# Kernel tuning notes

Measured on AMD Instinct MI355X. Metric: run time of the kernel, lower is better.

The kernel has to match this reference:

```python
import jax, jax.numpy as jnp
import numpy as np

N = 50000
E = 600000
D = 128
BN_EPS = 1e-5


def _gcn_layer(x, src, dst, ew, W, b, n):
    # x: [N, Din] -> [N, Dout]; PyG GCNConv: linear, symmetric norm (self-loops
    # already appended to src/dst/ew by caller), gather, scatter-add, bias.
    h = x @ W  # [N, Dout]
    deg = jax.ops.segment_sum(ew, dst, num_segments=n)  # [N]
    dinv = jnp.where(deg > 0, jax.lax.rsqrt(jnp.maximum(deg, 1e-30)), 0.0)
    norm = dinv[src] * ew * dinv[dst]  # [E+N]
    msg = h[src] * norm[:, None]  # [E+N, Dout] -- dominant memory traffic
    out = jax.ops.segment_sum(msg, dst, num_segments=n)
    return out + b


def _bn_eval(x, gamma, beta, mean, var):
    return (x - mean) * jax.lax.rsqrt(var + BN_EPS) * gamma + beta


def setup_inputs() -> dict:
    key = jax.random.key(0)
    ks = jax.random.split(key, 16)
    s = 1.0 / np.sqrt(D)
    inp = {
        "x": jax.random.normal(ks[0], (N, D), dtype=jnp.float32),
        "edge_index": jax.random.randint(ks[1], (2, E), 0, N, dtype=jnp.int32),
        "edge_weight": jax.random.uniform(ks[2], (E,), dtype=jnp.float32),
        "W0": jax.random.uniform(ks[3], (D, D), jnp.float32, -s, s),
        "b0": jnp.zeros((D,), jnp.float32),
        "W1": jax.random.uniform(ks[4], (D, D), jnp.float32, -s, s),
        "b1": jnp.zeros((D,), jnp.float32),
        "gamma0": jnp.ones((D,), jnp.float32),
        "beta0": jnp.zeros((D,), jnp.float32),
        "mean0": 0.1 * jax.random.normal(ks[5], (D,), jnp.float32),
        "var0": jax.random.uniform(ks[6], (D,), jnp.float32, 0.5, 1.5),
        "gamma1": jnp.ones((D,), jnp.float32),
        "beta1": jnp.zeros((D,), jnp.float32),
        "mean1": 0.1 * jax.random.normal(ks[7], (D,), jnp.float32),
        "var1": jax.random.uniform(ks[8], (D,), jnp.float32, 0.5, 1.5),
        "act_params": jnp.ones((2,), jnp.float32),  # activation_params init = ones(num_layers)
    }
    return inp


def reference(x, edge_index, edge_weight, W0, b0, W1, b1, gamma0, beta0, mean0, var0, gamma1, beta1, mean1, var1, act_params):
    # Add self-loops with weight 1 (PyG gcn_norm fill_value=1), shared by both layers.
    loop = jnp.arange(N, dtype=edge_index.dtype)
    src = jnp.concatenate([edge_index[0], loop])
    dst = jnp.concatenate([edge_index[1], loop])
    ew = jnp.concatenate([edge_weight, jnp.ones((N,), edge_weight.dtype)])

    # layer 0: conv -> BN (eval: running stats) -> adaptive ReLU/GELU blend
    h = _gcn_layer(x, src, dst, ew, W0, b0, N)
    h = _bn_eval(h, gamma0, beta0, mean0, var0)
    alpha = jax.nn.sigmoid(act_params[0])
    h = alpha * jax.nn.relu(h) + (1.0 - alpha) * jax.nn.gelu(h, approximate=False)
    # dropout: identity in eval mode

    # layer 1 (last): conv -> BN, no activation/dropout
    h = _gcn_layer(h, src, dst, ew, W1, b1, N)
    h = _bn_eval(h, gamma1, beta1, mean1, var1)
    return h
```

## Files before the change

### kernel.cpp

```cpp
#include <hip/hip_runtime.h>
#include <hip/hip_fp16.h>
#include <math.h>
#include <type_traits>

#define D 128
#define BN_EPS 1e-5f

typedef _Float16 half8 __attribute__((ext_vector_type(8)));
typedef float f32x4 __attribute__((ext_vector_type(4)));

__global__ void k_init(uint4* __restrict__ z, int n4,
                       const float* __restrict__ W0, const float* __restrict__ W1,
                       _Float16* __restrict__ p0, _Float16* __restrict__ p1, int Z) {
  if ((int)blockIdx.x < Z) {
    int i = blockIdx.x * 256 + threadIdx.x;
    if (i < n4) z[i] = make_uint4(0u, 0u, 0u, 0u);
    return;
  }
  const float* W = (blockIdx.x - Z) ? W1 : W0;
  _Float16* P = (blockIdx.x - Z) ? p1 : p0;
  for (int idx = threadIdx.x; idx < 32 * 64; idx += 256) {
    int ntks = idx >> 6;
    int lane = idx & 63;
    int nt = ntks >> 2, ks = ntks & 3;
    int kb = ks * 32 + (lane >> 4) * 8;
    int c = nt * 16 + (lane & 15);
#pragma unroll
    for (int i = 0; i < 8; ++i)
      P[(size_t)idx * 8 + i] = (_Float16)W[(size_t)(kb + i) * D + c];
  }
}

__global__ __launch_bounds__(256) void k_cnt_gemm0(const float* __restrict__ X,
                                                   const _Float16* __restrict__ Bp,
                                                   __half* __restrict__ H,
                                                   const int* __restrict__ dst,
                                                   int* cnt16, int* __restrict__ rank,
                                                   int n, int e, int Gc) {
  if ((int)blockIdx.x < Gc) {
    int base = blockIdx.x * 1024 + threadIdx.x;
#pragma unroll
    for (int jj = 0; jj < 4; ++jj) {
      int i = base + jj * 256;
      if (i < e) rank[i] = atomicAdd(&cnt16[(size_t)dst[i] * 16], 1);
    }
    return;
  }

  const int lane = threadIdx.x & 63;
  const int wave = threadIdx.x >> 6;
  const int r0 = (blockIdx.x - Gc) * 64 + wave * 16;
  const int arow = r0 + (lane & 15);
  const int kbase = (lane >> 4) * 8;
  const bool av = arow < n;

  f32x4 acc[8];
#pragma unroll
  for (int t = 0; t < 8; ++t) acc[t] = (f32x4){0.f, 0.f, 0.f, 0.f};

#pragma unroll
  for (int ks = 0; ks < 4; ++ks) {
    half8 a;
    if (av) {
      const float* ap = X + (size_t)arow * D + ks * 32 + kbase;
      float4 f0 = *(const float4*)ap;
      float4 f1 = *(const float4*)(ap + 4);
      a[0] = (_Float16)f0.x; a[1] = (_Float16)f0.y;
      a[2] = (_Float16)f0.z; a[3] = (_Float16)f0.w;
      a[4] = (_Float16)f1.x; a[5] = (_Float16)f1.y;
      a[6] = (_Float16)f1.z; a[7] = (_Float16)f1.w;
    } else {
#pragma unroll
      for (int i = 0; i < 8; ++i) a[i] = (_Float16)0.f;
    }
#pragma unroll
    for (int nt = 0; nt < 8; ++nt) {
      half8 b = *(const half8*)(Bp + ((size_t)(nt * 4 + ks) * 64 + lane) * 8);
      acc[nt] = __builtin_amdgcn_mfma_f32_16x16x32_f16(a, b, acc[nt], 0, 0, 0);
    }
  }

  const int rbase = (lane >> 4) * 4;
  const int col = lane & 15;
#pragma unroll
  for (int nt = 0; nt < 8; ++nt) {
#pragma unroll
    for (int j = 0; j < 4; ++j) {
      int rr = r0 + rbase + j;
      if (rr < n) H[(size_t)rr * D + nt * 16 + col] = __float2half(acc[nt][j]);
    }
  }
}

__global__ __launch_bounds__(1024) void k_scan1(const int* __restrict__ cnt16,
                                                int* __restrict__ off, int* bsum, int n) {
  __shared__ int ws[16];
  const int tid = threadIdx.x;
  const int i = blockIdx.x * 1024 + tid;
  int v = (i < n) ? cnt16[(size_t)i * 16] : 0;
  int x = v;
#pragma unroll
  for (int d = 1; d < 64; d <<= 1) {
    int y = __shfl_up(x, d, 64);
    if ((tid & 63) >= d) x += y;
  }
  const int wid = tid >> 6;
  if ((tid & 63) == 63) ws[wid] = x;
  __syncthreads();
  if (wid == 0) {
    int s = (tid < 16) ? ws[tid] : 0;
#pragma unroll
    for (int d = 1; d < 16; d <<= 1) {
      int y = __shfl_up(s, d, 64);
      if (tid >= d && tid < 16) s += y;
    }
    if (tid < 16) ws[tid] = s;
  }
  __syncthreads();
  int woff = (wid > 0) ? ws[wid - 1] : 0;
  if (i < n) off[i] = woff + x - v;
  if (tid == 1023) bsum[blockIdx.x] = ws[15];
}

__global__ __launch_bounds__(1024) void k_scan23(int* off, const int* __restrict__ bsum,
                                                 int n, int nb) {
  __shared__ int sh[2];
  const int tid = threadIdx.x;
  if (tid < 64) {
    int x = (tid < nb) ? bsum[tid] : 0;
#pragma unroll
    for (int d = 1; d < 64; d <<= 1) {
      int y = __shfl_up(x, d, 64);
      if (tid >= d) x += y;
    }
    int pfx = (blockIdx.x > 0) ? __shfl(x, (int)blockIdx.x - 1, 64) : 0;
    int tot = __shfl(x, nb - 1, 64);
    if (tid == 0) { sh[0] = pfx; sh[1] = tot; }
  }
  __syncthreads();
  const int i = blockIdx.x * 1024 + tid;
  if (i < n) off[i] += sh[0];
  if (blockIdx.x == 0 && tid == 0) off[n] = sh[1];
}

__global__ void k_bucket(const int* __restrict__ src, const int* __restrict__ dst,
                         const float* __restrict__ ew, const int* __restrict__ off,
                         const int* __restrict__ rank, uint2* __restrict__ pack, int e) {
  int i = blockIdx.x * blockDim.x + threadIdx.x;
  if (i < e) {
    int d = dst[i];
    int pos = off[d] + rank[i];
    pack[pos] = make_uint2((unsigned)src[i], __float_as_uint(ew[i]));
  }
}

__global__ void k_degdinv(const int* __restrict__ off, const uint2* __restrict__ pack,
                          float* __restrict__ dinv, int n) {
  int g = blockIdx.x * blockDim.x + threadIdx.x;
  if (g < n) {
    float deg = 1.0f;
    int k1 = off[g + 1];
    for (int k = off[g]; k < k1; ++k) deg += __uint_as_float(pack[k].y);
    dinv[g] = rsqrtf(deg);
  }
}

__device__ __forceinline__ void h8_to_f(const uint4& r, float* f) {
  const __half2* hp = (const __half2*)&r;
#pragma unroll
  for (int t = 0; t < 4; ++t) {
    float2 v = __half22float2(hp[t]);
    f[2 * t] = v.x; f[2 * t + 1] = v.y;
  }
}

template <bool ACT>
__device__ __forceinline__ void agg_node(const __half* __restrict__ H,
                                         const int* __restrict__ off,
                                         const uint2* __restrict__ pack,
                                         const float* __restrict__ dinv,
                                         const float* __restrict__ bias,
                                         const float* __restrict__ gamma,
                                         const float* __restrict__ beta,
                                         const float* __restrict__ mean,
                                         const float* __restrict__ var,
                                         float alpha, int g, int j, float* acc) {
#pragma unroll
  for (int t = 0; t < 8; ++t) acc[t] = 0.f;

  int k = off[g], k1 = off[g + 1];
  for (; k + 3 < k1; k += 4) {
    uint2 p0 = pack[k], p1 = pack[k + 1], p2 = pack[k + 2], p3 = pack[k + 3];
    float w0 = dinv[p0.x] * __uint_as_float(p0.y);
    float w1 = dinv[p1.x] * __uint_as_float(p1.y);
    float w2 = dinv[p2.x] * __uint_as_float(p2.y);
    float w3 = dinv[p3.x] * __uint_as_float(p3.y);
    uint4 r0 = *(const uint4*)(H + (size_t)p0.x * D + j);
    uint4 r1 = *(const uint4*)(H + (size_t)p1.x * D + j);
    uint4 r2 = *(const uint4*)(H + (size_t)p2.x * D + j);
    uint4 r3 = *(const uint4*)(H + (size_t)p3.x * D + j);
    float f0[8], f1[8], f2[8], f3[8];
    h8_to_f(r0, f0); h8_to_f(r1, f1); h8_to_f(r2, f2); h8_to_f(r3, f3);
#pragma unroll
    for (int t = 0; t < 8; ++t)
      acc[t] += w0 * f0[t] + w1 * f1[t] + w2 * f2[t] + w3 * f3[t];
  }
  for (; k < k1; ++k) {
    uint2 p = pack[k];
    float w = dinv[p.x] * __uint_as_float(p.y);
    uint4 r = *(const uint4*)(H + (size_t)p.x * D + j);
    float f[8];
    h8_to_f(r, f);
#pragma unroll
    for (int t = 0; t < 8; ++t) acc[t] += w * f[t];
  }

  float dg = dinv[g];
  uint4 rs = *(const uint4*)(H + (size_t)g * D + j);
  float fs[8];
  h8_to_f(rs, fs);
#pragma unroll
  for (int t = 0; t < 8; ++t) acc[t] = dg * acc[t] + dg * dg * fs[t];

  float bb[8], gm[8], bt[8], mn[8], vr[8];
  *(float4*)&bb[0] = *(const float4*)(bias + j);  *(float4*)&bb[4] = *(const float4*)(bias + j + 4);
  *(float4*)&gm[0] = *(const float4*)(gamma + j); *(float4*)&gm[4] = *(const float4*)(gamma + j + 4);
  *(float4*)&bt[0] = *(const float4*)(beta + j);  *(float4*)&bt[4] = *(const float4*)(beta + j + 4);
  *(float4*)&mn[0] = *(const float4*)(mean + j);  *(float4*)&mn[4] = *(const float4*)(mean + j + 4);
  *(float4*)&vr[0] = *(const float4*)(var + j);   *(float4*)&vr[4] = *(const float4*)(var + j + 4);

#pragma unroll
  for (int t = 0; t < 8; ++t) {
    float vv = (acc[t] + bb[t] - mn[t]) * rsqrtf(vr[t] + BN_EPS) * gm[t] + bt[t];
    if (ACT) {
      float rl = fmaxf(vv, 0.f);
      float ge = 0.5f * vv * (1.f + erff(vv * 0.70710678118654752f));
      vv = alpha * rl + (1.f - alpha) * ge;
    }
    acc[t] = vv;
  }
}

__global__ __launch_bounds__(256) void k_agg_gemm(const __half* __restrict__ H,
                                                  const int* __restrict__ off,
                                                  const uint2* __restrict__ pack,
                                                  const float* __restrict__ dinv,
                                                  const float* __restrict__ bias,
                                                  const float* __restrict__ gamma,
                                                  const float* __restrict__ beta,
                                                  const float* __restrict__ mean,
                                                  const float* __restrict__ var,
                                                  const float* __restrict__ act_params,
                                                  const _Float16* __restrict__ Bp,
                                                  __half* __restrict__ Hout, int n) {
  __shared__ _Float16 sA[32][136];
  const int tid = threadIdx.x;
  const int row0 = blockIdx.x * 32;
  const int grp = tid >> 4;
  const int j = (tid & 15) * 8;
  const float alpha = 1.f / (1.f + expf(-act_params[0]));

#pragma unroll
  for (int it = 0; it < 2; ++it) {
    int lr = it * 16 + grp;
    int g = row0 + lr;
    half8 st;
    if (g < n) {
      float acc[8];
      agg_node<true>(H, off, pack, dinv, bias, gamma, beta, mean, var, alpha, g, j, acc);
#pragma unroll
      for (int t = 0; t < 8; ++t) st[t] = (_Float16)acc[t];
    } else {
#pragma unroll
      for (int t = 0; t < 8; ++t) st[t] = (_Float16)0.f;
    }
    *(half8*)&sA[lr][j] = st;
  }
  __syncthreads();

  const int lane = tid & 63;
  const int wave = tid >> 6;
  const int lrow = (wave & 1) * 16;
  const int ntb = (wave >> 1) * 4;
  const int arowl = lrow + (lane & 15);
  const int kbase = (lane >> 4) * 8;

  f32x4 acc[4];
#pragma unroll
  for (int t = 0; t < 4; ++t) acc[t] = (f32x4){0.f, 0.f, 0.f, 0.f};

#pragma unroll
  for (int ks = 0; ks < 4; ++ks) {
    half8 a = *(const half8*)&sA[arowl][ks * 32 + kbase];
#pragma unroll
    for (int nt = 0; nt < 4; ++nt) {
      half8 b = *(const half8*)(Bp + ((size_t)((ntb + nt) * 4 + ks) * 64 + lane) * 8);
      acc[nt] = __builtin_amdgcn_mfma_f32_16x16x32_f16(a, b, acc[nt], 0, 0, 0);
    }
  }

  const int rbase = (lane >> 4) * 4;
  const int col = lane & 15;
#pragma unroll
  for (int nt = 0; nt < 4; ++nt) {
#pragma unroll
    for (int jj = 0; jj < 4; ++jj) {
      int rr = row0 + lrow + rbase + jj;
      if (rr < n) Hout[(size_t)rr * D + (ntb + nt) * 16 + col] = __float2half(acc[nt][jj]);
    }
  }
}

template <typename OutT, bool ACT>
__global__ __launch_bounds__(256) void k_agg(const __half* __restrict__ H,
                                             const int* __restrict__ off,
                                             const uint2* __restrict__ pack,
                                             const float* __restrict__ dinv,
                                             const float* __restrict__ bias,
                                             const float* __restrict__ gamma,
                                             const float* __restrict__ beta,
                                             const float* __restrict__ mean,
                                             const float* __restrict__ var,
                                             const float* __restrict__ act_params,
                                             OutT* __restrict__ out, int n) {
  int g = blockIdx.x * 16 + (threadIdx.x >> 4);
  if (g >= n) return;
  const int j = (threadIdx.x & 15) * 8;
  const float alpha = ACT ? 1.f / (1.f + expf(-act_params[0])) : 0.f;

  float acc[8];
  agg_node<ACT>(H, off, pack, dinv, bias, gamma, beta, mean, var, alpha, g, j, acc);

  if constexpr (std::is_same<OutT, __half>::value) {
    uint4 st;
    __half2* hp = (__half2*)&st;
    hp[0] = __floats2half2_rn(acc[0], acc[1]);
    hp[1] = __floats2half2_rn(acc[2], acc[3]);
    hp[2] = __floats2half2_rn(acc[4], acc[5]);
    hp[3] = __floats2half2_rn(acc[6], acc[7]);
    *(uint4*)(out + (size_t)g * D + j) = st;
  } else {
    *(float4*)(out + (size_t)g * D + j)     = make_float4(acc[0], acc[1], acc[2], acc[3]);
    *(float4*)(out + (size_t)g * D + j + 4) = make_float4(acc[4], acc[5], acc[6], acc[7]);
  }
}

extern "C" void kernel_launch(void* const* d_in, const int* in_sizes, int n_in,
                              void* d_out, int out_size, void* d_ws, size_t ws_size,
                              hipStream_t stream) {
  const float* x      = (const float*)d_in[0];
  const int*   ei     = (const int*)d_in[1];
  const float* ew     = (const float*)d_in[2];
  const float* W0     = (const float*)d_in[3];
  const float* b0     = (const float*)d_in[4];
  const float* W1     = (const float*)d_in[5];
  const float* b1     = (const float*)d_in[6];
  const float* gamma0 = (const float*)d_in[7];
  const float* beta0  = (const float*)d_in[8];
  const float* mean0  = (const float*)d_in[9];
  const float* var0   = (const float*)d_in[10];
  const float* gamma1 = (const float*)d_in[11];
  const float* beta1  = (const float*)d_in[12];
  const float* mean1  = (const float*)d_in[13];
  const float* var1   = (const float*)d_in[14];
  const float* act    = (const float*)d_in[15];

  const int n = in_sizes[0] / D;
  const int e = in_sizes[2];
  const int* srcp = ei;
  const int* dstp = ei + e;

  uintptr_t p = (uintptr_t)d_ws;
  auto carve = [&p](size_t bytes) -> void* {
    void* r = (void*)p;
    p += (bytes + 255) & ~(size_t)255;
    return r;
  };
  float*    dinv  = (float*)carve(sizeof(float) * n);
  int*      off   = (int*)carve(sizeof(int) * (n + 1));
  int*      rank  = (int*)carve(sizeof(int) * e);
  int*      bsum  = (int*)carve(sizeof(int) * 1024);
  int*      cnt16 = (int*)carve(sizeof(int) * (size_t)n * 16);
  _Float16* w0p   = (_Float16*)carve(sizeof(_Float16) * 32 * 64 * 8);
  _Float16* w1p   = (_Float16*)carve(sizeof(_Float16) * 32 * 64 * 8);
  uint2*    pack  = (uint2*)carve(sizeof(uint2) * e);
  __half*   h16   = (__half*)carve(sizeof(__half) * (size_t)n * D);
  __half*   h16b  = (__half*)carve(sizeof(__half) * (size_t)n * D);
  float*    out   = (float*)d_out;

  const int tpb = 256;
  const int nb_n = (n + tpb - 1) / tpb;
  const int nb_e = (e + tpb - 1) / tpb;
  const int nb_s = (n + 1023) / 1024;
  const int Gc   = (e + 1023) / 1024;
  const int Gg   = (n + 63) / 64;
  const int nz4  = n * 4;
  const int Z    = (nz4 + tpb - 1) / tpb;

  k_init<<<Z + 2, tpb, 0, stream>>>((uint4*)cnt16, nz4, W0, W1, w0p, w1p, Z);
  k_cnt_gemm0<<<Gc + Gg, tpb, 0, stream>>>(x, w0p, h16, dstp, cnt16, rank, n, e, Gc);
  k_scan1<<<nb_s, 1024, 0, stream>>>(cnt16, off, bsum, n);
  k_scan23<<<nb_s, 1024, 0, stream>>>(off, bsum, n, nb_s);
  k_bucket<<<nb_e, tpb, 0, stream>>>(srcp, dstp, ew, off, rank, pack, e);
  k_degdinv<<<nb_n, tpb, 0, stream>>>(off, pack, dinv, n);

  k_agg_gemm<<<(n + 31) / 32, tpb, 0, stream>>>(
      h16, off, pack, dinv, b0, gamma0, beta0, mean0, var0, act, w1p, h16b, n);

  k_agg<float, false><<<(n + 15) / 16, tpb, 0, stream>>>(
      h16b, off, pack, dinv, b1, gamma1, beta1, mean1, var1, act, out, n);
}
```

Before: 129.5 us.

## Cooperatively load edge lists via shuffles and halve agg_gemm rows per block

```diff
diff --git a/kernel.cpp b/kernel.cpp
--- a/kernel.cpp
+++ b/kernel.cpp
@@ -184,35 +184,33 @@
                                          const float* __restrict__ beta,
                                          const float* __restrict__ mean,
                                          const float* __restrict__ var,
-                                         float alpha, int g, int j, float* acc) {
+                                         float alpha, int g, int q, int j, float* acc) {
 #pragma unroll
   for (int t = 0; t < 8; ++t) acc[t] = 0.f;
 
-  int k = off[g], k1 = off[g + 1];
-  for (; k + 3 < k1; k += 4) {
-    uint2 p0 = pack[k], p1 = pack[k + 1], p2 = pack[k + 2], p3 = pack[k + 3];
-    float w0 = dinv[p0.x] * __uint_as_float(p0.y);
-    float w1 = dinv[p1.x] * __uint_as_float(p1.y);
-    float w2 = dinv[p2.x] * __uint_as_float(p2.y);
-    float w3 = dinv[p3.x] * __uint_as_float(p3.y);
-    uint4 r0 = *(const uint4*)(H + (size_t)p0.x * D + j);
-    uint4 r1 = *(const uint4*)(H + (size_t)p1.x * D + j);
-    uint4 r2 = *(const uint4*)(H + (size_t)p2.x * D + j);
-    uint4 r3 = *(const uint4*)(H + (size_t)p3.x * D + j);
-    float f0[8], f1[8], f2[8], f3[8];
-    h8_to_f(r0, f0); h8_to_f(r1, f1); h8_to_f(r2, f2); h8_to_f(r3, f3);
-#pragma unroll
-    for (int t = 0; t < 8; ++t)
-      acc[t] += w0 * f0[t] + w1 * f1[t] + w2 * f2[t] + w3 * f3[t];
-  }
-  for (; k < k1; ++k) {
-    uint2 p = pack[k];
-    float w = dinv[p.x] * __uint_as_float(p.y);
-    uint4 r = *(const uint4*)(H + (size_t)p.x * D + j);
-    float f[8];
-    h8_to_f(r, f);
-#pragma unroll
-    for (int t = 0; t < 8; ++t) acc[t] += w * f[t];
+  const int k0 = off[g], k1 = off[g + 1];
+  for (int kb = k0; kb < k1; kb += 16) {
+    int m = k1 - kb;
+    if (m > 16) m = 16;
+    unsigned sl = 0u;
+    float wl = 0.f;
+    if (q < m) {
+      uint2 pl = pack[kb + q];
+      sl = pl.x;
+      wl = dinv[pl.x] * __uint_as_float(pl.y);
+    }
+#pragma unroll
+    for (int t = 0; t < 16; ++t) {
+      if (t < m) {
+        unsigned s = (unsigned)__shfl((int)sl, t, 16);
+        float w = __shfl(wl, t, 16);
+        uint4 r = *(const uint4*)(H + (size_t)s * D + j);
+        float f[8];
+        h8_to_f(r, f);
+#pragma unroll
+        for (int u = 0; u < 8; ++u) acc[u] += w * f[u];
+      }
+    }
   }
 
   float dg = dinv[g];
@@ -253,47 +251,43 @@
                                                   const float* __restrict__ act_params,
                                                   const _Float16* __restrict__ Bp,
                                                   __half* __restrict__ Hout, int n) {
-  __shared__ _Float16 sA[32][136];
+  __shared__ _Float16 sA[16][136];
   const int tid = threadIdx.x;
-  const int row0 = blockIdx.x * 32;
+  const int row0 = blockIdx.x * 16;
   const int grp = tid >> 4;
-  const int j = (tid & 15) * 8;
+  const int q = tid & 15;
+  const int j = q * 8;
   const float alpha = 1.f / (1.f + expf(-act_params[0]));
 
-#pragma unroll
-  for (int it = 0; it < 2; ++it) {
-    int lr = it * 16 + grp;
-    int g = row0 + lr;
-    half8 st;
-    if (g < n) {
-      float acc[8];
-      agg_node<true>(H, off, pack, dinv, bias, gamma, beta, mean, var, alpha, g, j, acc);
-#pragma unroll
-      for (int t = 0; t < 8; ++t) st[t] = (_Float16)acc[t];
-    } else {
-#pragma unroll
-      for (int t = 0; t < 8; ++t) st[t] = (_Float16)0.f;
-    }
-    *(half8*)&sA[lr][j] = st;
-  }
+  const int g = row0 + grp;
+  half8 st;
+  if (g < n) {
+    float acc[8];
+    agg_node<true>(H, off, pack, dinv, bias, gamma, beta, mean, var, alpha, g, q, j, acc);
+#pragma unroll
+    for (int t = 0; t < 8; ++t) st[t] = (_Float16)acc[t];
+  } else {
+#pragma unroll
+    for (int t = 0; t < 8; ++t) st[t] = (_Float16)0.f;
+  }
+  *(half8*)&sA[grp][j] = st;
   __syncthreads();
 
   const int lane = tid & 63;
   const int wave = tid >> 6;
-  const int lrow = (wave & 1) * 16;
-  const int ntb = (wave >> 1) * 4;
-  const int arowl = lrow + (lane & 15);
+  const int ntb = wave * 2;
+  const int arowl = lane & 15;
   const int kbase = (lane >> 4) * 8;
 
-  f32x4 acc[4];
-#pragma unroll
-  for (int t = 0; t < 4; ++t) acc[t] = (f32x4){0.f, 0.f, 0.f, 0.f};
+  f32x4 acc[2];
+#pragma unroll
+  for (int t = 0; t < 2; ++t) acc[t] = (f32x4){0.f, 0.f, 0.f, 0.f};
 
 #pragma unroll
   for (int ks = 0; ks < 4; ++ks) {
     half8 a = *(const half8*)&sA[arowl][ks * 32 + kbase];
 #pragma unroll
-    for (int nt = 0; nt < 4; ++nt) {
+    for (int nt = 0; nt < 2; ++nt) {
       half8 b = *(const half8*)(Bp + ((size_t)((ntb + nt) * 4 + ks) * 64 + lane) * 8);
       acc[nt] = __builtin_amdgcn_mfma_f32_16x16x32_f16(a, b, acc[nt], 0, 0, 0);
     }
@@ -302,10 +296,10 @@
   const int rbase = (lane >> 4) * 4;
   const int col = lane & 15;
 #pragma unroll
-  for (int nt = 0; nt < 4; ++nt) {
+  for (int nt = 0; nt < 2; ++nt) {
 #pragma unroll
     for (int jj = 0; jj < 4; ++jj) {
-      int rr = row0 + lrow + rbase + jj;
+      int rr = row0 + rbase + jj;
       if (rr < n) Hout[(size_t)rr * D + (ntb + nt) * 16 + col] = __float2half(acc[nt][jj]);
     }
   }
@@ -325,11 +319,12 @@
                                              OutT* __restrict__ out, int n) {
   int g = blockIdx.x * 16 + (threadIdx.x >> 4);
   if (g >= n) return;
-  const int j = (threadIdx.x & 15) * 8;
+  const int q = threadIdx.x & 15;
+  const int j = q * 8;
   const float alpha = ACT ? 1.f / (1.f + expf(-act_params[0])) : 0.f;
 
   float acc[8];
-  agg_node<ACT>(H, off, pack, dinv, bias, gamma, beta, mean, var, alpha, g, j, acc);
+  agg_node<ACT>(H, off, pack, dinv, bias, gamma, beta, mean, var, alpha, g, q, j, acc);
 
   if constexpr (std::is_same<OutT, __half>::value) {
     uint4 st;
@@ -404,7 +399,7 @@
   k_bucket<<<nb_e, tpb, 0, stream>>>(srcp, dstp, ew, off, rank, pack, e);
   k_degdinv<<<nb_n, tpb, 0, stream>>>(off, pack, dinv, n);
 
-  k_agg_gemm<<<(n + 31) / 32, tpb, 0, stream>>>(
+  k_agg_gemm<<<(n + 15) / 16, tpb, 0, stream>>>(
       h16, off, pack, dinv, b0, gamma0, beta0, mean0, var0, act, w1p, h16b, n);
 
   k_agg<float, false><<<(n + 15) / 16, tpb, 0, stream>>>(
```

After: 129.5 us. Within noise of the previous version (+0.1%).
